# Optimization experiments

Measured on AMD Instinct MI355X. Metric: run time of the kernel, lower is better.

The kernel has to match this reference:

```python
import jax, jax.numpy as jnp
import numpy as np

B, F, T = 4, 2048, 2048
CF, CT = 1024, 1024
H, DH = 16, 64
ALPHA = 1.0 / np.sqrt(DH).astype(np.float32)


def setup_inputs() -> dict:
    key = jax.random.key(0)
    ks = jax.random.split(key, 8)
    s = 0.02  # trunc_normal-ish init scale
    return {
        "from_tensor": jax.random.normal(ks[0], (B, F, CF), jnp.float32),
        "to_tensor": jax.random.normal(ks[1], (B, T, CT), jnp.float32),
        "mask": jax.random.randint(ks[2], (B, F, T), 0, 2, jnp.int32),
        "Wq": jax.random.normal(ks[3], (CF, H * DH), jnp.float32) * s,
        "bq": jnp.zeros((H * DH,), jnp.float32),
        "Wk": jax.random.normal(ks[4], (CT, H * DH), jnp.float32) * s,
        "bk": jnp.zeros((H * DH,), jnp.float32),
        "Wv": jax.random.normal(ks[5], (CT, H * DH), jnp.float32) * s,
        "bv": jnp.zeros((H * DH,), jnp.float32),
    }


def reference(from_tensor, to_tensor, mask, Wq, bq, Wk, bk, Wv, bv):
    # projections (nn.Linear with no activation)
    q = from_tensor @ Wq + bq          # [B,F,H*DH]
    k = to_tensor @ Wk + bk            # [B,T,H*DH]
    v = to_tensor @ Wv + bv            # [B,T,H*DH]
    q = q.reshape(B, F, H, DH)         # query: [..., F, H, DH]
    k = k.reshape(B, T, DH, H)         # key:   [..., T, DH, H]  (self._shape[::-1])
    v = v.reshape(B, T, H, DH)
    # score = transpose(q,-3,-2) @ transpose(k,-3,-1) * alpha -> [B,H,F,T]
    score = jnp.einsum("bfhd,btdh->bhft", q, k) * ALPHA
    if mask is not None:
        adder = (1.0 - mask[:, None].astype(score.dtype)) * -100000.0  # [B,1,F,T]
        score = score + adder
    probs = jax.nn.softmax(score, axis=-1)  # dropout p=0.0 -> identity
    # context = probs @ transpose(v,-3,-2), then transpose back: [B,F,H,DH]
    context = jnp.einsum("bhft,bthd->bfhd", probs, v)
    return context.reshape(B, F, H * DH)
```

## Files before the change

### kernel.cpp

```cpp
#include <hip/hip_runtime.h>
#include <type_traits>

typedef __bf16 bf16_t;
typedef __attribute__((ext_vector_type(8))) __bf16 bf16x8;
typedef __attribute__((ext_vector_type(4))) float f32x4;
typedef __attribute__((ext_vector_type(16))) float f32x16;

__device__ __forceinline__ void async16(const void* g, void* lds) {
  __builtin_amdgcn_global_load_lds((const __attribute__((address_space(1))) unsigned int*)g,
                                   (__attribute__((address_space(3))) unsigned int*)lds, 16, 0, 0);
}

__device__ __forceinline__ unsigned pk2(float lo, float hi) {
  unsigned short a = __builtin_bit_cast(unsigned short, (__bf16)lo);
  unsigned short b = __builtin_bit_cast(unsigned short, (__bf16)hi);
  return (unsigned)a | ((unsigned)b << 16);
}

__device__ __forceinline__ void plswap(unsigned& a, unsigned& b) {
#if __has_builtin(__builtin_amdgcn_permlane32_swap)
  auto r = __builtin_amdgcn_permlane32_swap((int)a, (int)b, false, false);
  a = (unsigned)r[0];
  b = (unsigned)r[1];
#else
  const bool hb = (threadIdx.x & 32) != 0;
  unsigned bx = (unsigned)__shfl_xor((int)b, 32);
  unsigned ax = (unsigned)__shfl_xor((int)a, 32);
  unsigned na = hb ? bx : a;
  unsigned nb = hb ? b : ax;
  a = na; b = nb;
#endif
}

__global__ __launch_bounds__(256) void pack_mask_kernel(const int* __restrict__ mask,
                                                        unsigned long long* __restrict__ mb) {
  const int lane = threadIdx.x & 63, w = threadIdx.x >> 6;
  for (int i = 0; i < 32; ++i) {
    size_t word = (size_t)blockIdx.x * 128 + (size_t)i * 4 + w;
    unsigned long long bits = __ballot(mask[word * 64 + lane] != 0);
    if (lane == 0) mb[word] = bits;
  }
}

__global__ __launch_bounds__(256) void cvt_bf16_kernel(const float* __restrict__ in, bf16_t* __restrict__ out) {
  size_t i = (size_t)blockIdx.x * 256 + threadIdx.x;
  const float4* in4 = (const float4*)in;
  float4 a = in4[i * 2], b = in4[i * 2 + 1];
  bf16x8 o;
  o[0] = (__bf16)a.x; o[1] = (__bf16)a.y; o[2] = (__bf16)a.z; o[3] = (__bf16)a.w;
  o[4] = (__bf16)b.x; o[5] = (__bf16)b.y; o[6] = (__bf16)b.z; o[7] = (__bf16)b.w;
  *(bf16x8*)(out + i * 8) = o;
}

__global__ __launch_bounds__(256) void wt_cvt_kernel(const float* __restrict__ Wq, const float* __restrict__ Wk,
                                                     const float* __restrict__ Wv, bf16_t* __restrict__ Wt) {
  const int z = blockIdx.z;
  const float* src = (z == 0) ? Wq : ((z == 1) ? Wk : Wv);
  const float sc = (z == 0) ? 0.18033688011112042f : 1.0f;
  bf16_t* dst = Wt + (size_t)z * 1024 * 1024;
  const int n = blockIdx.x * 64 + (threadIdx.x & 63);
  const int k8 = blockIdx.y * 4 + (threadIdx.x >> 6);
  bf16x8 o;
#pragma unroll
  for (int j = 0; j < 8; ++j) o[j] = (__bf16)(src[(size_t)(k8 * 8 + j) * 1024 + n] * sc);
  *(bf16x8*)(dst + (size_t)n * 1024 + k8 * 8) = o;
}

__global__ __launch_bounds__(256) void proj_kernel(const bf16_t* __restrict__ A, const bf16_t* __restrict__ Wt,
                                                   const float* __restrict__ bias, bf16_t* __restrict__ dst,
                                                   const int z, const float bscale) {
  __shared__ __align__(16) unsigned char smem[33792];
  bf16_t* se = (bf16_t*)smem;
  const int tid = threadIdx.x, lane = tid & 63, w = tid >> 6;
  const int m0 = blockIdx.x * 128, n0 = blockIdx.y * 128;
  const int wm = (w >> 1) * 64, wn = (w & 1) * 64;
  const int r = lane & 15, kq = lane >> 4;
  const int srow = lane >> 2, sslot = lane & 3;
  f32x4 acc[4][4] = {};

  auto stage = [&](int buf, int k0) {
    bf16_t* Ad = se + buf * 4096;
    bf16_t* Bd = se + 8192 + buf * 4096;
#pragma unroll
    for (int it = 0; it < 2; ++it) {
      const int c = it * 4 + w;
      const int row = c * 16 + srow;
      async16(A + (size_t)(m0 + row) * 1024 + k0 + ((sslot ^ (row & 3)) * 8), Ad + c * 512);
      async16(Wt + (size_t)(n0 + row) * 1024 + k0 + ((sslot ^ (row & 3)) * 8), Bd + c * 512);
    }
  };

  stage(0, 0);
  __syncthreads();
  for (int tile = 0; tile < 32; ++tile) {
    const int cur = tile & 1;
    if (tile < 31) stage(cur ^ 1, (tile + 1) * 32);
    const bf16_t* Al = se + cur * 4096;
    const bf16_t* Bl = se + 8192 + cur * 4096;
    bf16x8 af[4], bfr[4];
#pragma unroll
    for (int i = 0; i < 4; ++i) {
      const int ra = wm + i * 16 + r;
      af[i] = *(const bf16x8*)(Al + ra * 32 + ((kq ^ (ra & 3)) * 8));
      const int rb = wn + i * 16 + r;
      bfr[i] = *(const bf16x8*)(Bl + rb * 32 + ((kq ^ (rb & 3)) * 8));
    }
    __builtin_amdgcn_s_setprio(1);
#pragma unroll
    for (int i = 0; i < 4; ++i)
#pragma unroll
      for (int j = 0; j < 4; ++j)
        acc[i][j] = __builtin_amdgcn_mfma_f32_16x16x32_bf16(af[i], bfr[j], acc[i][j], 0, 0, 0);
    __builtin_amdgcn_s_setprio(0);
    __syncthreads();
  }

  bf16_t* Cl = se;
  float bvv[4];
#pragma unroll
  for (int j = 0; j < 4; ++j) bvv[j] = bias[n0 + wn + j * 16 + r] * bscale;
#pragma unroll
  for (int i = 0; i < 4; ++i)
#pragma unroll
    for (int j = 0; j < 4; ++j)
#pragma unroll
      for (int g = 0; g < 4; ++g)
        Cl[(wm + i * 16 + kq * 4 + g) * 132 + wn + j * 16 + r] = (__bf16)(acc[i][j][g] + bvv[j]);
  __syncthreads();

  const int b = m0 >> 11, sbase = m0 & 2047;
  if (z == 0) {
#pragma unroll
    for (int q = 0; q < 8; ++q) {
      const int cid = q * 256 + tid;
      const int m = cid >> 4, c = (cid >> 3) & 1, d8 = cid & 7;
      bf16x8 val = *(const bf16x8*)(Cl + m * 132 + c * 64 + d8 * 8);
      *(bf16x8*)(dst + ((size_t)(b * 16 + (n0 >> 6) + c) * 2048 + sbase + m) * 64 + d8 * 8) = val;
    }
  } else if (z == 1) {
#pragma unroll
    for (int q = 0; q < 8; ++q) {
      const int cid = q * 256 + tid;
      const int hh = cid >> 7, m = cid & 127;
      bf16x8 val;
#pragma unroll
      for (int dd = 0; dd < 8; ++dd) val[dd] = Cl[m * 132 + dd * 16 + hh];
      *(bf16x8*)(dst + ((size_t)(b * 16 + hh) * 2048 + sbase + m) * 64 + (n0 >> 4)) = val;
    }
  } else {
#pragma unroll
    for (int q = 0; q < 8; ++q) {
      const int cid = q * 256 + tid;
      const int nl = cid >> 4, m8 = cid & 15;
      bf16x8 val;
#pragma unroll
      for (int s = 0; s < 8; ++s) val[s] = Cl[(m8 * 8 + s) * 132 + nl];
      const int hh = (n0 >> 6) + (nl >> 6), dd = nl & 63;
      *(bf16x8*)(dst + ((size_t)(b * 16 + hh) * 64 + dd) * 2048 + sbase + m8 * 8) = val;
    }
  }
}

__global__ __launch_bounds__(256, 2) void attn_kernel(const bf16_t* __restrict__ Q, const bf16_t* __restrict__ K,
                                                      const bf16_t* __restrict__ VT,
                                                      const unsigned long long* __restrict__ mb,
                                                      float* __restrict__ out) {
  __shared__ __align__(16) unsigned char smem[32768];
  bf16_t* se = (bf16_t*)smem;
  const int tid = threadIdx.x, lane = tid & 63, w = tid >> 6;
  const int cl = lane & 31, hi = lane >> 5;

  const int lid = blockIdx.x + 8 * (blockIdx.y + 16 * blockIdx.z);
  const int xcd = lid & 7, q_ = lid >> 3;
  const int pairIdx = xcd * 8 + (q_ & 7);
  const int f0 = (q_ >> 3) * 256;
  const int h = pairIdx & 15, b = pairIdx >> 4;

  const size_t bh = (size_t)b * 16 + h;
  const int fw = f0 + w * 64;

  const bf16_t* Qb = Q + (bh * 2048 + fw) * 64;
  bf16x8 qf[2][4];
#pragma unroll
  for (int fb = 0; fb < 2; ++fb)
#pragma unroll
    for (int ks = 0; ks < 4; ++ks)
      qf[fb][ks] = *(const bf16x8*)(Qb + (fb * 32 + cl) * 64 + ks * 16 + hi * 8);

  f32x16 Of[2][2] = {};
  float lacc[2] = {0.f, 0.f};
  bf16x8 paw[2][4];

  const unsigned long long* mrow[2];
  mrow[0] = mb + ((size_t)b * 2048 + fw + cl) * 32;
  mrow[1] = mb + ((size_t)b * 2048 + fw + 32 + cl) * 32;

  const int row8 = lane >> 3, slot = lane & 7;
  const int swz = (slot ^ row8) * 8;
  const bf16_t* kgb[2];
  const bf16_t* vgb[2];
#pragma unroll
  for (int it = 0; it < 2; ++it) {
    const int row = it * 32 + w * 8 + row8;
    kgb[it] = K + (bh * 2048 + row) * 64 + swz;
    vgb[it] = VT + (bh * 64 + row) * 2048 + swz;
  }

  auto stage_k = [&](int buf, int tile) {
    bf16_t* kd = se + buf * 4096 + w * 512;
#pragma unroll
    for (int it = 0; it < 2; ++it)
      async16(kgb[it] + (size_t)tile * 4096, kd + it * 2048);
  };
  auto stage_v = [&](int buf, int tile) {
    bf16_t* vd = se + 8192 + buf * 4096 + w * 512;
#pragma unroll
    for (int it = 0; it < 2; ++it)
      async16(vgb[it] + (size_t)tile * 64, vd + it * 2048);
  };

  auto pv_step = [&](int vbuf) {
    const bf16_t* Vl = se + 8192 + vbuf * 4096;
    __builtin_amdgcn_s_setprio(1);
#pragma unroll
    for (int db = 0; db < 2; ++db) {
      const int vrow0 = db * 32 + cl;
#pragma unroll
      for (int kt = 0; kt < 4; ++kt) {
        bf16x8 vf = *(const bf16x8*)(Vl + vrow0 * 64 + (((2 * kt + hi) ^ (vrow0 & 7)) * 8));
        Of[0][db] = __builtin_amdgcn_mfma_f32_32x32x16_bf16(paw[0][kt], vf, Of[0][db], 0, 0, 0);
        Of[1][db] = __builtin_amdgcn_mfma_f32_32x32x16_bf16(paw[1][kt], vf, Of[1][db], 0, 0, 0);
      }
    }
    __builtin_amdgcn_s_setprio(0);
  };

  unsigned long long mA[2], mB[2];
  stage_k(0, 0);
  mA[0] = mrow[0][0];
  mA[1] = mrow[1][0];
  __syncthreads();

  auto body = [&](auto curc, auto dopvc, unsigned long long (&mc)[2], unsigned long long (&mn)[2], int tile) {
    constexpr int cur = decltype(curc)::value;
    constexpr bool dopv = decltype(dopvc)::value;
    if (tile < 31) {
      stage_k(cur ^ 1, tile + 1);
      mn[0] = mrow[0][tile + 1];
      mn[1] = mrow[1][tile + 1];
    }
    stage_v(cur, tile);
    const bf16_t* Kl = se + cur * 4096;

    f32x16 st0[2], st1[2];
#pragma unroll
    for (int fb = 0; fb < 2; ++fb) {
      const unsigned mw0 = (unsigned)(mc[fb] >> (4 * hi));
      const unsigned mw1 = (unsigned)(mc[fb] >> (32 + 4 * hi));
#pragma unroll
      for (int q = 0; q < 4; ++q)
#pragma unroll
        for (int e = 0; e < 4; ++e) {
          const int idx = q * 4 + e;
          const int pos = e + 8 * q;
          const unsigned s0 = (unsigned)(((int)(mw0 << (31 - pos))) >> 31);
          const unsigned s1 = (unsigned)(((int)(mw1 << (31 - pos))) >> 31);
          st0[fb][idx] = __uint_as_float(~s0 & 0xC6EA6000u);
          st1[fb][idx] = __uint_as_float(~s1 & 0xC6EA6000u);
        }
    }

    {
      const int krow = cl;
      __builtin_amdgcn_s_setprio(1);
#pragma unroll
      for (int ks = 0; ks < 4; ++ks) {
        bf16x8 kf = *(const bf16x8*)(Kl + krow * 64 + (((2 * ks + hi) ^ (krow & 7)) * 8));
        st0[0] = __builtin_amdgcn_mfma_f32_32x32x16_bf16(kf, qf[0][ks], st0[0], 0, 0, 0);
        st0[1] = __builtin_amdgcn_mfma_f32_32x32x16_bf16(kf, qf[1][ks], st0[1], 0, 0, 0);
      }
      __builtin_amdgcn_s_setprio(0);
    }

    if constexpr (dopv) pv_step(cur ^ 1);

    {
      const int krow = 32 + cl;
      __builtin_amdgcn_s_setprio(1);
#pragma unroll
      for (int ks = 0; ks < 4; ++ks) {
        bf16x8 kf = *(const bf16x8*)(Kl + krow * 64 + (((2 * ks + hi) ^ (krow & 7)) * 8));
        st1[0] = __builtin_amdgcn_mfma_f32_32x32x16_bf16(kf, qf[0][ks], st1[0], 0, 0, 0);
        st1[1] = __builtin_amdgcn_mfma_f32_32x32x16_bf16(kf, qf[1][ks], st1[1], 0, 0, 0);
      }
      __builtin_amdgcn_s_setprio(0);
    }

#pragma unroll
    for (int ts = 0; ts < 2; ++ts) {
#pragma unroll
      for (int fb = 0; fb < 2; ++fb) {
        const f32x16& stf = (ts == 0) ? st0[fb] : st1[fb];
        float pv[16];
#pragma unroll
        for (int q = 0; q < 4; ++q)
#pragma unroll
          for (int e = 0; e < 4; ++e) {
            const int idx = q * 4 + e;
            float p = __builtin_amdgcn_exp2f(stf[idx]);
            lacc[fb] += p;
            pv[idx] = p;
          }
#pragma unroll
        for (int kl = 0; kl < 2; ++kl) {
          const int qa = 2 * kl, qb = qa + 1;
          unsigned x0 = pk2(pv[qa * 4 + 0], pv[qa * 4 + 1]);
          unsigned y0 = pk2(pv[qb * 4 + 0], pv[qb * 4 + 1]);
          unsigned x1 = pk2(pv[qa * 4 + 2], pv[qa * 4 + 3]);
          unsigned y1 = pk2(pv[qb * 4 + 2], pv[qb * 4 + 3]);
          plswap(x0, y0);
          plswap(x1, y1);
          union { unsigned u[4]; bf16x8 v; } tmp;
          tmp.u[0] = x0; tmp.u[1] = x1; tmp.u[2] = y0; tmp.u[3] = y1;
          paw[fb][ts * 2 + kl] = tmp.v;
        }
      }
    }
    __syncthreads();
  };

  using c0 = std::integral_constant<int, 0>;
  using c1 = std::integral_constant<int, 1>;
  using bF = std::integral_constant<bool, false>;
  using bT = std::integral_constant<bool, true>;

  body(c0{}, bF{}, mA, mB, 0);
  body(c1{}, bT{}, mB, mA, 1);
  for (int tile = 2; tile < 32; tile += 2) {
    body(c0{}, bT{}, mA, mB, tile);
    body(c1{}, bT{}, mB, mA, tile + 1);
  }
  pv_step(1);

#pragma unroll
  for (int fb = 0; fb < 2; ++fb) lacc[fb] += __shfl_xor(lacc[fb], 32);
  float* lsh = (float*)smem;
  if (hi == 0) {
    lsh[w * 64 + cl] = lacc[0];
    lsh[w * 64 + 32 + cl] = lacc[1];
  }
#pragma unroll
  for (int fb = 0; fb < 2; ++fb)
#pragma unroll
    for (int q = 0; q < 4; ++q)
#pragma unroll
      for (int e = 0; e < 4; ++e) {
        const int idx = q * 4 + e;
        const int row = e + 8 * q + 4 * hi;
        const float li = 1.0f / lsh[w * 64 + fb * 32 + row];
        const size_t orow = ((size_t)b * 2048 + fw + fb * 32 + row) * 1024 + h * 64;
        out[orow + cl] = Of[fb][0][idx] * li;
        out[orow + 32 + cl] = Of[fb][1][idx] * li;
      }
}

extern "C" void kernel_launch(void* const* d_in, const int* in_sizes, int n_in,
                              void* d_out, int out_size, void* d_ws, size_t ws_size,
                              hipStream_t stream) {
  (void)in_sizes; (void)n_in; (void)out_size; (void)ws_size;
  const float* from = (const float*)d_in[0];
  const float* to_  = (const float*)d_in[1];
  const int*   mask = (const int*)d_in[2];
  const float* Wq = (const float*)d_in[3];
  const float* bq = (const float*)d_in[4];
  const float* Wk = (const float*)d_in[5];
  const float* bk = (const float*)d_in[6];
  const float* Wv = (const float*)d_in[7];
  const float* bv = (const float*)d_in[8];
  float* out = (float*)d_out;
  char* ws = (char*)d_ws;

  bf16_t* Qw = (bf16_t*)(ws);
  bf16_t* Kw = (bf16_t*)(ws + (size_t)(1u << 24));
  bf16_t* Vw = (bf16_t*)(ws + (size_t)(2u << 24));
  bf16_t* Wt = (bf16_t*)(ws + (size_t)(3u << 24));
  unsigned long long* mbits = (unsigned long long*)(ws + (size_t)(3u << 24) + (size_t)(6u << 20));
  bf16_t* inb = (bf16_t*)(ws + (size_t)(3u << 24) + (size_t)(8u << 20));

  pack_mask_kernel<<<2048, 256, 0, stream>>>(mask, mbits);
  wt_cvt_kernel<<<dim3(16, 32, 3), 256, 0, stream>>>(Wq, Wk, Wv, Wt);
  cvt_bf16_kernel<<<4096, 256, 0, stream>>>(from, inb);
  proj_kernel<<<dim3(64, 8), 256, 0, stream>>>(inb, Wt, bq, Qw, 0, 0.18033688011112042f);
  cvt_bf16_kernel<<<4096, 256, 0, stream>>>(to_, inb);
  proj_kernel<<<dim3(64, 8), 256, 0, stream>>>(inb, Wt + (1u << 20), bk, Kw, 1, 1.0f);
  proj_kernel<<<dim3(64, 8), 256, 0, stream>>>(inb, Wt + (2u << 20), bv, Vw, 2, 1.0f);
  attn_kernel<<<dim3(8, 16, 4), 256, 0, stream>>>(Qw, Kw, Vw, mbits, out);
}
```

Before: 218.0 us.

## Fuse prep kernels, batch projections in one launch, 4-stage attention pipeline

Merges the mask packing, weight transpose/convert and both input bf16 conversions into one prep kernel. The three projection GEMMs now run as a single grid with z selecting Q/K/V, and the to_tensor bf16 copy is staged in the output buffer. The attention kernel moves from double-buffered K with synchronous V staging to a 4-deep ring of K and V buffers, using explicit vmcnt waits and one barrier per tile instead of a trailing __syncthreads. This aims to cut launch overhead, fill the GPU better during projections, and hide load latency, at the cost of doubling LDS to 64KB, which may reduce occupancy.

```diff
diff --git a/kernel.cpp b/kernel.cpp
--- a/kernel.cpp
+++ b/kernel.cpp
@@ -32,45 +32,59 @@
 #endif
 }
 
-__global__ __launch_bounds__(256) void pack_mask_kernel(const int* __restrict__ mask,
-                                                        unsigned long long* __restrict__ mb) {
-  const int lane = threadIdx.x & 63, w = threadIdx.x >> 6;
-  for (int i = 0; i < 32; ++i) {
-    size_t word = (size_t)blockIdx.x * 128 + (size_t)i * 4 + w;
-    unsigned long long bits = __ballot(mask[word * 64 + lane] != 0);
-    if (lane == 0) mb[word] = bits;
-  }
-}
-
-__global__ __launch_bounds__(256) void cvt_bf16_kernel(const float* __restrict__ in, bf16_t* __restrict__ out) {
-  size_t i = (size_t)blockIdx.x * 256 + threadIdx.x;
-  const float4* in4 = (const float4*)in;
-  float4 a = in4[i * 2], b = in4[i * 2 + 1];
-  bf16x8 o;
-  o[0] = (__bf16)a.x; o[1] = (__bf16)a.y; o[2] = (__bf16)a.z; o[3] = (__bf16)a.w;
-  o[4] = (__bf16)b.x; o[5] = (__bf16)b.y; o[6] = (__bf16)b.z; o[7] = (__bf16)b.w;
-  *(bf16x8*)(out + i * 8) = o;
-}
-
-__global__ __launch_bounds__(256) void wt_cvt_kernel(const float* __restrict__ Wq, const float* __restrict__ Wk,
-                                                     const float* __restrict__ Wv, bf16_t* __restrict__ Wt) {
-  const int z = blockIdx.z;
-  const float* src = (z == 0) ? Wq : ((z == 1) ? Wk : Wv);
-  const float sc = (z == 0) ? 0.18033688011112042f : 1.0f;
-  bf16_t* dst = Wt + (size_t)z * 1024 * 1024;
-  const int n = blockIdx.x * 64 + (threadIdx.x & 63);
-  const int k8 = blockIdx.y * 4 + (threadIdx.x >> 6);
-  bf16x8 o;
-#pragma unroll
-  for (int j = 0; j < 8; ++j) o[j] = (__bf16)(src[(size_t)(k8 * 8 + j) * 1024 + n] * sc);
-  *(bf16x8*)(dst + (size_t)n * 1024 + k8 * 8) = o;
-}
-
-__global__ __launch_bounds__(256) void proj_kernel(const bf16_t* __restrict__ A, const bf16_t* __restrict__ Wt,
-                                                   const float* __restrict__ bias, bf16_t* __restrict__ dst,
-                                                   const int z, const float bscale) {
+__global__ __launch_bounds__(256) void prep_kernel(const int* __restrict__ mask, unsigned long long* __restrict__ mb,
+                                                   const float* __restrict__ Wq, const float* __restrict__ Wk,
+                                                   const float* __restrict__ Wv, bf16_t* __restrict__ Wt,
+                                                   const float* __restrict__ from, bf16_t* __restrict__ inbF,
+                                                   const float* __restrict__ to_, bf16_t* __restrict__ inbT) {
+  const int bid = blockIdx.x, tid = threadIdx.x;
+  if (bid < 2048) {
+    const int lane = tid & 63, w = tid >> 6;
+    for (int i = 0; i < 32; ++i) {
+      size_t word = (size_t)bid * 128 + (size_t)i * 4 + w;
+      unsigned long long bits = __ballot(mask[word * 64 + lane] != 0);
+      if (lane == 0) mb[word] = bits;
+    }
+  } else if (bid < 3584) {
+    const int idx = bid - 2048;
+    const int z = idx >> 9, r = idx & 511;
+    const float* src = (z == 0) ? Wq : ((z == 1) ? Wk : Wv);
+    const float sc = (z == 0) ? 0.18033688011112042f : 1.0f;
+    bf16_t* dst = Wt + (size_t)z * 1024 * 1024;
+    const int n = (r & 15) * 64 + (tid & 63);
+    const int k8 = (r >> 4) * 4 + (tid >> 6);
+    bf16x8 o;
+#pragma unroll
+    for (int j = 0; j < 8; ++j) o[j] = (__bf16)(src[(size_t)(k8 * 8 + j) * 1024 + n] * sc);
+    *(bf16x8*)(dst + (size_t)n * 1024 + k8 * 8) = o;
+  } else {
+    const bool isF = bid < 7680;
+    const size_t i = (size_t)(bid - (isF ? 3584 : 7680)) * 256 + tid;
+    const float4* in4 = (const float4*)(isF ? from : to_);
+    bf16_t* outp = isF ? inbF : inbT;
+    float4 a = in4[i * 2], b = in4[i * 2 + 1];
+    bf16x8 o;
+    o[0] = (__bf16)a.x; o[1] = (__bf16)a.y; o[2] = (__bf16)a.z; o[3] = (__bf16)a.w;
+    o[4] = (__bf16)b.x; o[5] = (__bf16)b.y; o[6] = (__bf16)b.z; o[7] = (__bf16)b.w;
+    *(bf16x8*)(outp + i * 8) = o;
+  }
+}
+
+__global__ __launch_bounds__(256) void proj_kernel(const bf16_t* __restrict__ inbF, const bf16_t* __restrict__ inbT,
+                                                   const bf16_t* __restrict__ Wt,
+                                                   const float* __restrict__ bq, const float* __restrict__ bk,
+                                                   const float* __restrict__ bv,
+                                                   bf16_t* __restrict__ Qw, bf16_t* __restrict__ Kw,
+                                                   bf16_t* __restrict__ Vw) {
   __shared__ __align__(16) unsigned char smem[33792];
   bf16_t* se = (bf16_t*)smem;
+  const int z = blockIdx.z;
+  const bf16_t* A = (z == 0) ? inbF : inbT;
+  const bf16_t* Wz = Wt + (size_t)z * 1024 * 1024;
+  const float* bias = (z == 0) ? bq : ((z == 1) ? bk : bv);
+  bf16_t* dst = (z == 0) ? Qw : ((z == 1) ? Kw : Vw);
+  const float bscale = (z == 0) ? 0.18033688011112042f : 1.0f;
+
   const int tid = threadIdx.x, lane = tid & 63, w = tid >> 6;
   const int m0 = blockIdx.x * 128, n0 = blockIdx.y * 128;
   const int wm = (w >> 1) * 64, wn = (w & 1) * 64;
@@ -86,7 +100,7 @@
       const int c = it * 4 + w;
       const int row = c * 16 + srow;
       async16(A + (size_t)(m0 + row) * 1024 + k0 + ((sslot ^ (row & 3)) * 8), Ad + c * 512);
-      async16(Wt + (size_t)(n0 + row) * 1024 + k0 + ((sslot ^ (row & 3)) * 8), Bd + c * 512);
+      async16(Wz + (size_t)(n0 + row) * 1024 + k0 + ((sslot ^ (row & 3)) * 8), Bd + c * 512);
     }
   };
 
@@ -165,7 +179,7 @@
                                                       const bf16_t* __restrict__ VT,
                                                       const unsigned long long* __restrict__ mb,
                                                       float* __restrict__ out) {
-  __shared__ __align__(16) unsigned char smem[32768];
+  __shared__ __align__(16) unsigned char smem[65536];
   bf16_t* se = (bf16_t*)smem;
   const int tid = threadIdx.x, lane = tid & 63, w = tid >> 6;
   const int cl = lane & 31, hi = lane >> 5;
@@ -213,14 +227,14 @@
       async16(kgb[it] + (size_t)tile * 4096, kd + it * 2048);
   };
   auto stage_v = [&](int buf, int tile) {
-    bf16_t* vd = se + 8192 + buf * 4096 + w * 512;
+    bf16_t* vd = se + 16384 + buf * 4096 + w * 512;
 #pragma unroll
     for (int it = 0; it < 2; ++it)
       async16(vgb[it] + (size_t)tile * 64, vd + it * 2048);
   };
 
-  auto pv_step = [&](int vbuf) {
-    const bf16_t* Vl = se + 8192 + vbuf * 4096;
+  auto pv_step = [&](int vs) {
+    const bf16_t* Vl = se + 16384 + vs * 4096;
     __builtin_amdgcn_s_setprio(1);
 #pragma unroll
     for (int db = 0; db < 2; ++db) {
@@ -235,38 +249,45 @@
     __builtin_amdgcn_s_setprio(0);
   };
 
-  unsigned long long mA[2], mB[2];
-  stage_k(0, 0);
-  mA[0] = mrow[0][0];
-  mA[1] = mrow[1][0];
-  __syncthreads();
-
-  auto body = [&](auto curc, auto dopvc, unsigned long long (&mc)[2], unsigned long long (&mn)[2], int tile) {
-    constexpr int cur = decltype(curc)::value;
-    constexpr bool dopv = decltype(dopvc)::value;
-    if (tile < 31) {
-      stage_k(cur ^ 1, tile + 1);
-      mn[0] = mrow[0][tile + 1];
-      mn[1] = mrow[1][tile + 1];
-    }
-    stage_v(cur, tile);
-    const bf16_t* Kl = se + cur * 4096;
+  unsigned long long m[4][2];
+  stage_k(0, 0); stage_v(0, 0);
+  stage_k(1, 1); stage_v(1, 1);
+  m[0][0] = mrow[0][0];
+  m[0][1] = mrow[1][0];
+
+  auto body = [&](auto Sc, auto lastc, int tile) {
+    constexpr int S = decltype(Sc)::value;
+    constexpr bool last = decltype(lastc)::value;
+    if constexpr (last) {
+      asm volatile("s_waitcnt vmcnt(0)" ::: "memory");
+    } else {
+      asm volatile("s_waitcnt vmcnt(6)" ::: "memory");
+    }
+    __builtin_amdgcn_s_barrier();
+    __builtin_amdgcn_sched_barrier(0);
+    if (tile + 2 < 32) {
+      stage_k((S + 2) & 3, tile + 2);
+      stage_v((S + 2) & 3, tile + 2);
+    }
+    if (tile + 1 < 32) {
+      m[(S + 1) & 3][0] = mrow[0][tile + 1];
+      m[(S + 1) & 3][1] = mrow[1][tile + 1];
+    }
+    const bf16_t* Kl = se + S * 4096;
 
     f32x16 st0[2], st1[2];
 #pragma unroll
     for (int fb = 0; fb < 2; ++fb) {
-      const unsigned mw0 = (unsigned)(mc[fb] >> (4 * hi));
-      const unsigned mw1 = (unsigned)(mc[fb] >> (32 + 4 * hi));
+      const unsigned nm0 = ~((unsigned)(m[S][fb] >> (4 * hi)));
+      const unsigned nm1 = ~((unsigned)(m[S][fb] >> (32 + 4 * hi)));
 #pragma unroll
       for (int q = 0; q < 4; ++q)
 #pragma unroll
         for (int e = 0; e < 4; ++e) {
           const int idx = q * 4 + e;
           const int pos = e + 8 * q;
-          const unsigned s0 = (unsigned)(((int)(mw0 << (31 - pos))) >> 31);
-          const unsigned s1 = (unsigned)(((int)(mw1 << (31 - pos))) >> 31);
-          st0[fb][idx] = __uint_as_float(~s0 & 0xC6EA6000u);
-          st1[fb][idx] = __uint_as_float(~s1 & 0xC6EA6000u);
+          st0[fb][idx] = __uint_as_float(((unsigned)(((int)(nm0 << (31 - pos))) >> 31)) & 0xC6EA6000u);
+          st1[fb][idx] = __uint_as_float(((unsigned)(((int)(nm1 << (31 - pos))) >> 31)) & 0xC6EA6000u);
         }
     }
 
@@ -282,7 +303,7 @@
       __builtin_amdgcn_s_setprio(0);
     }
 
-    if constexpr (dopv) pv_step(cur ^ 1);
+    if (tile > 0) pv_step((S + 3) & 3);
 
     {
       const int krow = 32 + cl;
@@ -326,21 +347,26 @@
         }
       }
     }
-    __syncthreads();
   };
 
-  using c0 = std::integral_constant<int, 0>;
-  using c1 = std::integral_constant<int, 1>;
+  using s0 = std::integral_constant<int, 0>;
+  using s1 = std::integral_constant<int, 1>;
+  using s2 = std::integral_constant<int, 2>;
+  using s3 = std::integral_constant<int, 3>;
   using bF = std::integral_constant<bool, false>;
   using bT = std::integral_constant<bool, true>;
 
-  body(c0{}, bF{}, mA, mB, 0);
-  body(c1{}, bT{}, mB, mA, 1);
-  for (int tile = 2; tile < 32; tile += 2) {
-    body(c0{}, bT{}, mA, mB, tile);
-    body(c1{}, bT{}, mB, mA, tile + 1);
-  }
-  pv_step(1);
+  for (int t = 0; t < 28; t += 4) {
+    body(s0{}, bF{}, t);
+    body(s1{}, bF{}, t + 1);
+    body(s2{}, bF{}, t + 2);
+    body(s3{}, bF{}, t + 3);
+  }
+  body(s0{}, bF{}, 28);
+  body(s1{}, bF{}, 29);
+  body(s2{}, bF{}, 30);
+  body(s3{}, bT{}, 31);
+  pv_step(3);
 
 #pragma unroll
   for (int fb = 0; fb < 2; ++fb) lacc[fb] += __shfl_xor(lacc[fb], 32);
@@ -385,14 +411,10 @@
   bf16_t* Vw = (bf16_t*)(ws + (size_t)(2u << 24));
   bf16_t* Wt = (bf16_t*)(ws + (size_t)(3u << 24));
   unsigned long long* mbits = (unsigned long long*)(ws + (size_t)(3u << 24) + (size_t)(6u << 20));
-  bf16_t* inb = (bf16_t*)(ws + (size_t)(3u << 24) + (size_t)(8u << 20));
-
-  pack_mask_kernel<<<2048, 256, 0, stream>>>(mask, mbits);
-  wt_cvt_kernel<<<dim3(16, 32, 3), 256, 0, stream>>>(Wq, Wk, Wv, Wt);
-  cvt_bf16_kernel<<<4096, 256, 0, stream>>>(from, inb);
-  proj_kernel<<<dim3(64, 8), 256, 0, stream>>>(inb, Wt, bq, Qw, 0, 0.18033688011112042f);
-  cvt_bf16_kernel<<<4096, 256, 0, stream>>>(to_, inb);
-  proj_kernel<<<dim3(64, 8), 256, 0, stream>>>(inb, Wt + (1u << 20), bk, Kw, 1, 1.0f);
-  proj_kernel<<<dim3(64, 8), 256, 0, stream>>>(inb, Wt + (2u << 20), bv, Vw, 2, 1.0f);
+  bf16_t* inbF = (bf16_t*)(ws + (size_t)(3u << 24) + (size_t)(8u << 20));
+  bf16_t* inbT = (bf16_t*)d_out;
+
+  prep_kernel<<<11776, 256, 0, stream>>>(mask, mbits, Wq, Wk, Wv, Wt, from, inbF, to_, inbT);
+  proj_kernel<<<dim3(64, 8, 3), 256, 0, stream>>>(inbF, inbT, Wt, bq, bk, bv, Qw, Kw, Vw);
   attn_kernel<<<dim3(8, 16, 4), 256, 0, stream>>>(Qw, Kw, Vw, mbits, out);
 }
```

Result: faster. 206.6 us (-5.2%).
